# Kernel optimization log

Hardware: AMD Instinct MI355X
Metric: run time of the kernel (lower is better)

The kernel has to match this reference:

```python
import jax, jax.numpy as jnp
import numpy as np

N, P, D_IN, K, D_H = 4, 20000, 1024, 8, 64


def setup_inputs() -> dict:
    key = jax.random.key(0)
    ks = jax.random.split(key, 10)
    inp = {
        "x": jax.random.normal(ks[0], (N, P, D_IN), dtype=jnp.float32),
        "centroids": jax.random.normal(ks[1], (K, D_IN), dtype=jnp.float32),
        # proj_pre: Linear(in_dim, 64) + ReLU  (W stored as [in, out])
        "W_pre": jax.random.normal(ks[2], (D_IN, D_H), dtype=jnp.float32) / np.sqrt(D_IN),
        "b_pre": jnp.zeros((D_H,), dtype=jnp.float32),
        # attention: Linear(64,32) -> Tanh -> Linear(32,1)
        "W_a1": jax.random.normal(ks[3], (D_H, 32), dtype=jnp.float32) / np.sqrt(D_H),
        "b_a1": jnp.zeros((32,), dtype=jnp.float32),
        "W_a2": jax.random.normal(ks[4], (32, 1), dtype=jnp.float32) / np.sqrt(32.0),
        "b_a2": jnp.zeros((1,), dtype=jnp.float32),
        # proj_out: Linear(64,32) + ReLU (+ Dropout, identity at eval)
        "W_out": jax.random.normal(ks[5], (D_H, 32), dtype=jnp.float32) / np.sqrt(D_H),
        "b_out": jnp.zeros((32,), dtype=jnp.float32),
    }
    return inp


def reference(x, centroids, W_pre, b_pre, W_a1, b_a1, W_a2, b_a2, W_out, b_out):
    # --- cdist-based hard cluster assignment ---------------------------------
    # ||x - c||: use the expanded form to avoid an [n,p,K,d] broadcast.
    x2 = jnp.sum(x * x, axis=-1)                       # [n, p]
    c2 = jnp.sum(centroids * centroids, axis=-1)       # [K]
    d2 = x2[..., None] + c2 - 2.0 * jnp.einsum('npd,kd->npk', x, centroids)
    dist = jnp.sqrt(jnp.maximum(d2, 0.0))              # [n, p, K]

    wc = jax.nn.softmax(1e7 / dist, axis=-1)           # softmax(1e7/dist)
    wc = (wc > 0.5).astype(x.dtype)                    # hard assignment
    # F.normalize(p=1, dim=1): divide by per-(n,K) patch count (eps=1e-12)
    wc = wc / jnp.maximum(jnp.sum(wc, axis=1, keepdims=True), 1e-12)
    mask = jnp.sum(wc, axis=1) == 0                    # [n, K] empty clusters

    # --- per-patch projection -------------------------------------------------
    xp = jax.nn.relu(x @ W_pre + b_pre)                # [n, p, 64]

    # --- cluster pooling + attention ------------------------------------------
    x_cls = jnp.einsum('npd,nph->nhd', xp, wc)         # [n, K, 64]
    A = (jnp.tanh(x_cls @ W_a1 + b_a1) @ W_a2 + b_a2)[..., 0]  # [n, K]
    A = jnp.where(mask, jnp.asarray(-100000.0, A.dtype), A)
    wa = jax.nn.softmax(A, axis=-1)                    # [n, K]
    pooled = jnp.einsum('nhd,nh->nd', x_cls, wa)       # [n, 64]

    enc_cls = jax.nn.relu(pooled @ W_out + b_out)      # [n, 32] (dropout = eval)
    enc_seq = xp.reshape(-1, xp.shape[-1])             # [(n*p), 64]
    return enc_cls, enc_seq, enc_seq
```

## Files before the change

kernel.cpp:

```cpp
#include <hip/hip_runtime.h>
#include <math.h>

#define N_  4
#define P_  20000
#define DIN 1024
#define K_  8
#define DH  64
#define BP  128
#define NT  5

typedef float  f32x4 __attribute__((ext_vector_type(4)));
typedef short  s16x8 __attribute__((ext_vector_type(8)));
typedef unsigned int u32x4 __attribute__((ext_vector_type(4)));
typedef unsigned short ushort_t;


union FragU { u32x4 u; s16x8 s; };

__global__ __launch_bounds__(256) void k_prep(const float* __restrict__ W_pre,
                                              const float* __restrict__ centroids,
                                              float* __restrict__ ws) {
  const int c = blockIdx.x;
  const int t = threadIdx.x;
  ushort_t* Bth = (ushort_t*)(ws + 4096);
  ushort_t* Btl = (ushort_t*)(ws + 45056);
  for (int d = t; d < DIN; d += 256) {
    float v = 0.f;
    if (c < 64)      v = W_pre[(size_t)d * DH + c];
    else if (c < 72) v = centroids[(size_t)(c - 64) * DIN + d];
    unsigned u = __float_as_uint(v);
    unsigned r = u + 0x7FFFu + ((u >> 16) & 1u);
    unsigned hb = r & 0xFFFF0000u;
    float lo = v - __uint_as_float(hb);
    unsigned ul = __float_as_uint(lo);
    unsigned rl = ul + 0x7FFFu + ((ul >> 16) & 1u);
    Bth[(size_t)c * DIN + d] = (ushort_t)(hb >> 16);
    Btl[(size_t)c * DIN + d] = (ushort_t)(rl >> 16);
  }
}

__global__ __launch_bounds__(512) void k_init2(const float* __restrict__ centroids,
                                               float* __restrict__ ws) {
  const int t = threadIdx.x;
  int* gcnt = (int*)(ws + 2048);
  for (int i = t; i < N_ * K_ * DH; i += 512) ws[i] = 0.f;
  if (t < N_ * K_) gcnt[t] = 0;
  const int w = t >> 6, lane = t & 63;
  float s = 0.f;
  for (int d = lane; d < DIN; d += 64) {
    float v = centroids[(size_t)w * DIN + d];
    s += v * v;
  }
  for (int off = 32; off > 0; off >>= 1) s += __shfl_down(s, off, 64);
  if (lane == 0) ws[2080 + w] = s;
}

__global__ __launch_bounds__(256) void k_main(
    const float* __restrict__ x, const float* __restrict__ b_pre,
    float* __restrict__ out1, float* __restrict__ out2, float* __restrict__ ws) {
  __shared__ float xt[BP * 68];
  __shared__ float sc[BP * 9];
  __shared__ int   assign_s[BP];
  __shared__ int   cnt8[K_];
  __shared__ float c2s[K_];

  const int t = threadIdx.x;
  const int w = t >> 6, l = t & 63;
  const int n = blockIdx.y;
  const int p0 = blockIdx.x * BP;
  const int validP = (P_ - p0) < BP ? (P_ - p0) : BP;

  const ushort_t* Bth = (const ushort_t*)(ws + 4096);
  const ushort_t* Btl = (const ushort_t*)(ws + 45056);

  if (t < K_) { cnt8[t] = 0; c2s[t] = ws[2080 + t]; }

  f32x4 acc[2][NT];
#pragma unroll
  for (int rg = 0; rg < 2; ++rg)
#pragma unroll
    for (int tl = 0; tl < NT; ++tl) acc[rg][tl] = (f32x4){0.f, 0.f, 0.f, 0.f};

  const float* xbase = x + (size_t)n * P_ * DIN;
  const int quad8 = (l >> 4) << 3;

  for (int ch = 0; ch < 16; ++ch) {
    const int d0 = ch * 64;
    __syncthreads();
#pragma unroll
    for (int i = 0; i < 8; ++i) {
      const int idx = t + 256 * i;
      const int row = idx >> 4, c4 = (idx & 15) << 2;
      int gp = p0 + row; gp = gp < P_ ? gp : P_ - 1;
      f32x4 v = *(const f32x4*)(xbase + (size_t)gp * DIN + d0 + c4);
      *(f32x4*)(xt + row * 68 + c4) = v;
    }
    __syncthreads();

#pragma unroll
    for (int kk = 0; kk < 2; ++kk) {
      const int kb = d0 + kk * 32 + quad8;
      FragU bh[NT], bl[NT];
#pragma unroll
      for (int tl = 0; tl < NT; ++tl) {
        const size_t off = (size_t)(tl * 16 + (l & 15)) * DIN + kb;
        bh[tl].u = *(const u32x4*)(Bth + off);
        bl[tl].u = *(const u32x4*)(Btl + off);
      }
#pragma unroll
      for (int rg = 0; rg < 2; ++rg) {
        const int row = 32 * w + 16 * rg + (l & 15);
        const float* ap = xt + row * 68 + kk * 32 + quad8;
        f32x4 a0 = *(const f32x4*)ap;
        f32x4 a1 = *(const f32x4*)(ap + 4);
        float f[8];
#pragma unroll
        for (int e = 0; e < 4; ++e) { f[e] = a0[e]; f[4 + e] = a1[e]; }
        FragU ah, al;
#pragma unroll
        for (int q = 0; q < 4; ++q) {
          const unsigned u0 = __float_as_uint(f[2 * q]);
          const unsigned u1 = __float_as_uint(f[2 * q + 1]);
          ah.u[q] = (u0 >> 16) | (u1 & 0xFFFF0000u);
          const float l0 = f[2 * q]     - __uint_as_float(u0 & 0xFFFF0000u);
          const float l1 = f[2 * q + 1] - __uint_as_float(u1 & 0xFFFF0000u);
          al.u[q] = (__float_as_uint(l0) >> 16) | (__float_as_uint(l1) & 0xFFFF0000u);
        }
#pragma unroll
        for (int tl = 0; tl < NT; ++tl) {
          acc[rg][tl] = __builtin_amdgcn_mfma_f32_16x16x32_bf16(ah.s, bh[tl].s, acc[rg][tl], 0, 0, 0);
          acc[rg][tl] = __builtin_amdgcn_mfma_f32_16x16x32_bf16(ah.s, bl[tl].s, acc[rg][tl], 0, 0, 0);
          acc[rg][tl] = __builtin_amdgcn_mfma_f32_16x16x32_bf16(al.s, bh[tl].s, acc[rg][tl], 0, 0, 0);
        }
      }
    }
  }
  __syncthreads();

#pragma unroll
  for (int tl = 0; tl < 4; ++tl) {
    const int col = tl * 16 + (l & 15);
    const float bb = b_pre[col];
#pragma unroll
    for (int rg = 0; rg < 2; ++rg) {
#pragma unroll
      for (int r = 0; r < 4; ++r) {
        const int row = 32 * w + 16 * rg + ((l >> 4) << 2) + r;
        float v = acc[rg][tl][r] + bb;
        v = v > 0.f ? v : 0.f;
        xt[row * 65 + col] = v;
        if (row < validP) {
          const size_t o = (((size_t)(n * P_ + p0 + row)) << 6) + col;
          out1[o] = v;
          out2[o] = v;
        }
      }
    }
  }
  if ((l & 15) < K_) {
    const int k = l & 15;
#pragma unroll
    for (int rg = 0; rg < 2; ++rg)
#pragma unroll
      for (int r = 0; r < 4; ++r) {
        const int row = 32 * w + 16 * rg + ((l >> 4) << 2) + r;
        sc[row * 9 + k] = c2s[k] - 2.f * acc[rg][4][r];
      }
  }
  __syncthreads();

  if (t < BP) {
    int a = -1;
    if (t < validP) {
      float best = 3.4e38f; int bk = 0;
#pragma unroll
      for (int k = 0; k < K_; ++k) {
        const float v = sc[t * 9 + k];
        if (v < best) { best = v; bk = k; }
      }
      a = bk;
      atomicAdd(&cnt8[bk], 1);
    }
    assign_s[t] = a;
  }
  __syncthreads();

  for (int task = t; task < K_ * DH; task += 256) {
    const int k = task >> 6, j = task & 63;
    float s = 0.f;
    for (int p = 0; p < BP; ++p)
      s += (assign_s[p] == k) ? xt[p * 65 + j] : 0.f;
    if (s != 0.f) atomicAdd(&ws[(n * K_ + k) * DH + j], s);
  }
  if (t < K_ && cnt8[t] > 0) atomicAdd((int*)(ws + 2048) + n * K_ + t, cnt8[t]);
}

__global__ __launch_bounds__(256) void k_final(
    const float* __restrict__ W_a1, const float* __restrict__ b_a1,
    const float* __restrict__ W_a2, const float* __restrict__ b_a2,
    const float* __restrict__ W_out, const float* __restrict__ b_out,
    const float* __restrict__ ws, float* __restrict__ enc_cls) {
  __shared__ float xc[N_ * K_ * DH];
  __shared__ float wa[N_ * K_];
  __shared__ float As[N_ * K_];
  __shared__ int   cnts[N_ * K_];
  __shared__ float pooled[N_ * DH];
  const int t = threadIdx.x;
  const float* gsum = ws;
  const int* gcnt = (const int*)(ws + 2048);

  if (t < N_ * K_) cnts[t] = gcnt[t];
  __syncthreads();
  for (int i = t; i < N_ * K_ * DH; i += 256) {
    const int nk = i >> 6;
    const int c = cnts[nk];
    xc[i] = (c > 0) ? gsum[i] / (float)c : 0.f;
  }
  __syncthreads();
  if (t < N_ * K_) {
    float a = b_a2[0];
    for (int h = 0; h < 32; ++h) {
      float z = b_a1[h];
      for (int j = 0; j < DH; ++j) z += xc[t * DH + j] * W_a1[j * 32 + h];
      a += tanhf(z) * W_a2[h];
    }
    As[t] = (cnts[t] > 0) ? a : -100000.f;
  }
  __syncthreads();
  if (t < N_) {
    float m = -3.4e38f;
    for (int k = 0; k < K_; ++k) m = fmaxf(m, As[t * K_ + k]);
    float ssum = 0.f;
    float e[K_];
    for (int k = 0; k < K_; ++k) { e[k] = expf(As[t * K_ + k] - m); ssum += e[k]; }
    for (int k = 0; k < K_; ++k) wa[t * K_ + k] = e[k] / ssum;
  }
  __syncthreads();
  {
    const int n = t >> 6, j = t & 63;
    float s = 0.f;
    for (int k = 0; k < K_; ++k) s += xc[(n * K_ + k) * DH + j] * wa[n * K_ + k];
    pooled[t] = s;
  }
  __syncthreads();
  if (t < N_ * 32) {
    const int n = t >> 5, o = t & 31;
    float s = b_out[o];
    for (int j = 0; j < DH; ++j) s += pooled[n * DH + j] * W_out[j * 32 + o];
    enc_cls[n * 32 + o] = fmaxf(s, 0.f);
  }
}

extern "C" void kernel_launch(void* const* d_in, const int* in_sizes, int n_in,
                              void* d_out, int out_size, void* d_ws, size_t ws_size,
                              hipStream_t stream) {
  const float* x         = (const float*)d_in[0];
  const float* centroids = (const float*)d_in[1];
  const float* W_pre     = (const float*)d_in[2];
  const float* b_pre     = (const float*)d_in[3];
  const float* W_a1      = (const float*)d_in[4];
  const float* b_a1      = (const float*)d_in[5];
  const float* W_a2      = (const float*)d_in[6];
  const float* b_a2      = (const float*)d_in[7];
  const float* W_out     = (const float*)d_in[8];
  const float* b_out     = (const float*)d_in[9];

  float* out     = (float*)d_out;
  float* ws      = (float*)d_ws;
  float* enc_cls = out;
  float* out1    = out + N_ * 32;
  float* out2    = out + N_ * 32 + (size_t)N_ * P_ * DH;

  hipLaunchKernelGGL(k_prep, dim3(80), dim3(256), 0, stream, W_pre, centroids, ws);
  hipLaunchKernelGGL(k_init2, dim3(1), dim3(512), 0, stream, centroids, ws);
  hipLaunchKernelGGL(k_main, dim3((P_ + BP - 1) / BP, N_), dim3(256), 0, stream,
                     x, b_pre, out1, out2, ws);
  hipLaunchKernelGGL(k_final, dim3(1), dim3(256), 0, stream,
                     W_a1, b_a1, W_a2, b_a2, W_out, b_out, ws, enc_cls);
}
```

Before: 620.1 us.

## Double-buffer x tiles via async global-to-LDS loads with XOR swizzle

The main kernel now stages each 64-column chunk of x into shared memory with global_load_lds direct copies into two alternating buffers. The next chunk is issued before the MFMA work on the current one, so global loads overlap compute and the register round trip plus one barrier per chunk go away. The padded layout is replaced by an XOR swizzle to avoid LDS bank conflicts. The two small setup kernels are also merged into one launch. Correctness depends on the barrier waiting for the outstanding LDS-DMA loads, and the doubled shared-memory footprint may lower occupancy.

New measurement: 589.6 us. 1.05x faster.

```diff
diff --git a/kernel.cpp b/kernel.cpp
--- a/kernel.cpp
+++ b/kernel.cpp
@@ -17,48 +17,53 @@
 
 union FragU { u32x4 u; s16x8 s; };
 
-__global__ __launch_bounds__(256) void k_prep(const float* __restrict__ W_pre,
-                                              const float* __restrict__ centroids,
-                                              float* __restrict__ ws) {
-  const int c = blockIdx.x;
+__device__ __forceinline__ void async_ld16(const float* g, float* l) {
+  __builtin_amdgcn_global_load_lds(
+      (const __attribute__((address_space(1))) unsigned int*)g,
+      (__attribute__((address_space(3))) unsigned int*)l, 16, 0, 0);
+}
+
+__global__ __launch_bounds__(512) void k_pre(const float* __restrict__ W_pre,
+                                             const float* __restrict__ centroids,
+                                             float* __restrict__ ws) {
   const int t = threadIdx.x;
-  ushort_t* Bth = (ushort_t*)(ws + 4096);
-  ushort_t* Btl = (ushort_t*)(ws + 45056);
-  for (int d = t; d < DIN; d += 256) {
-    float v = 0.f;
-    if (c < 64)      v = W_pre[(size_t)d * DH + c];
-    else if (c < 72) v = centroids[(size_t)(c - 64) * DIN + d];
-    unsigned u = __float_as_uint(v);
-    unsigned r = u + 0x7FFFu + ((u >> 16) & 1u);
-    unsigned hb = r & 0xFFFF0000u;
-    float lo = v - __uint_as_float(hb);
-    unsigned ul = __float_as_uint(lo);
-    unsigned rl = ul + 0x7FFFu + ((ul >> 16) & 1u);
-    Bth[(size_t)c * DIN + d] = (ushort_t)(hb >> 16);
-    Btl[(size_t)c * DIN + d] = (ushort_t)(rl >> 16);
-  }
-}
-
-__global__ __launch_bounds__(512) void k_init2(const float* __restrict__ centroids,
-                                               float* __restrict__ ws) {
-  const int t = threadIdx.x;
-  int* gcnt = (int*)(ws + 2048);
-  for (int i = t; i < N_ * K_ * DH; i += 512) ws[i] = 0.f;
-  if (t < N_ * K_) gcnt[t] = 0;
-  const int w = t >> 6, lane = t & 63;
-  float s = 0.f;
-  for (int d = lane; d < DIN; d += 64) {
-    float v = centroids[(size_t)w * DIN + d];
-    s += v * v;
-  }
-  for (int off = 32; off > 0; off >>= 1) s += __shfl_down(s, off, 64);
-  if (lane == 0) ws[2080 + w] = s;
+  const int b = blockIdx.x;
+  if (b < 80) {
+    const int c = b;
+    ushort_t* Bth = (ushort_t*)(ws + 4096);
+    ushort_t* Btl = (ushort_t*)(ws + 45056);
+    for (int d = t; d < DIN; d += 512) {
+      float v = 0.f;
+      if (c < 64)      v = W_pre[(size_t)d * DH + c];
+      else if (c < 72) v = centroids[(size_t)(c - 64) * DIN + d];
+      unsigned u = __float_as_uint(v);
+      unsigned r = u + 0x7FFFu + ((u >> 16) & 1u);
+      unsigned hb = r & 0xFFFF0000u;
+      float lo = v - __uint_as_float(hb);
+      unsigned ul = __float_as_uint(lo);
+      unsigned rl = ul + 0x7FFFu + ((ul >> 16) & 1u);
+      Bth[(size_t)c * DIN + d] = (ushort_t)(hb >> 16);
+      Btl[(size_t)c * DIN + d] = (ushort_t)(rl >> 16);
+    }
+  } else {
+    int* gcnt = (int*)(ws + 2048);
+    for (int i = t; i < N_ * K_ * DH; i += 512) ws[i] = 0.f;
+    if (t < N_ * K_) gcnt[t] = 0;
+    const int w = t >> 6, lane = t & 63;
+    float s = 0.f;
+    for (int d = lane; d < DIN; d += 64) {
+      float v = centroids[(size_t)w * DIN + d];
+      s += v * v;
+    }
+    for (int off = 32; off > 0; off >>= 1) s += __shfl_down(s, off, 64);
+    if (lane == 0) ws[2080 + w] = s;
+  }
 }
 
 __global__ __launch_bounds__(256) void k_main(
     const float* __restrict__ x, const float* __restrict__ b_pre,
     float* __restrict__ out1, float* __restrict__ out2, float* __restrict__ ws) {
-  __shared__ float xt[BP * 68];
+  __shared__ float smem[2 * BP * 64];
   __shared__ float sc[BP * 9];
   __shared__ int   assign_s[BP];
   __shared__ int   cnt8[K_];
@@ -66,6 +71,8 @@
 
   const int t = threadIdx.x;
   const int w = t >> 6, l = t & 63;
+  const int m = l & 15, q4 = l >> 4;
+  const int quad8 = q4 << 3;
   const int n = blockIdx.y;
   const int p0 = blockIdx.x * BP;
   const int validP = (P_ - p0) < BP ? (P_ - p0) : BP;
@@ -82,37 +89,48 @@
     for (int tl = 0; tl < NT; ++tl) acc[rg][tl] = (f32x4){0.f, 0.f, 0.f, 0.f};
 
   const float* xbase = x + (size_t)n * P_ * DIN;
-  const int quad8 = (l >> 4) << 3;
+
+  const float* gsrc[8];
+  float* ldst[8];
+#pragma unroll
+  for (int ii = 0; ii < 8; ++ii) {
+    const int R = w * 32 + ii * 4;
+    const int row = R + q4;
+    const int g = m ^ (row & 15);
+    int gp = p0 + row; gp = gp < P_ ? gp : P_ - 1;
+    gsrc[ii] = xbase + (size_t)gp * DIN + 4 * g;
+    ldst[ii] = smem + R * 64;
+  }
+
+#pragma unroll
+  for (int ii = 0; ii < 8; ++ii) async_ld16(gsrc[ii], ldst[ii]);
 
   for (int ch = 0; ch < 16; ++ch) {
-    const int d0 = ch * 64;
     __syncthreads();
-#pragma unroll
-    for (int i = 0; i < 8; ++i) {
-      const int idx = t + 256 * i;
-      const int row = idx >> 4, c4 = (idx & 15) << 2;
-      int gp = p0 + row; gp = gp < P_ ? gp : P_ - 1;
-      f32x4 v = *(const f32x4*)(xbase + (size_t)gp * DIN + d0 + c4);
-      *(f32x4*)(xt + row * 68 + c4) = v;
-    }
-    __syncthreads();
+    if (ch < 15) {
+      const int nb = (ch + 1) & 1;
+#pragma unroll
+      for (int ii = 0; ii < 8; ++ii)
+        async_ld16(gsrc[ii] + (ch + 1) * 64, ldst[ii] + nb * 8192);
+    }
+    const float* bufp = smem + (ch & 1) * 8192;
 
 #pragma unroll
     for (int kk = 0; kk < 2; ++kk) {
-      const int kb = d0 + kk * 32 + quad8;
+      const int kb = ch * 64 + kk * 32 + quad8;
       FragU bh[NT], bl[NT];
 #pragma unroll
       for (int tl = 0; tl < NT; ++tl) {
-        const size_t off = (size_t)(tl * 16 + (l & 15)) * DIN + kb;
+        const size_t off = (size_t)(tl * 16 + m) * DIN + kb;
         bh[tl].u = *(const u32x4*)(Bth + off);
         bl[tl].u = *(const u32x4*)(Btl + off);
       }
 #pragma unroll
       for (int rg = 0; rg < 2; ++rg) {
-        const int row = 32 * w + 16 * rg + (l & 15);
-        const float* ap = xt + row * 68 + kk * 32 + quad8;
-        f32x4 a0 = *(const f32x4*)ap;
-        f32x4 a1 = *(const f32x4*)(ap + 4);
+        const int row = 32 * w + 16 * rg + m;
+        const int ga = kk * 8 + (q4 << 1);
+        f32x4 a0 = *(const f32x4*)(bufp + row * 64 + 4 * (ga ^ m));
+        f32x4 a1 = *(const f32x4*)(bufp + row * 64 + 4 * ((ga + 1) ^ m));
         float f[8];
 #pragma unroll
         for (int e = 0; e < 4; ++e) { f[e] = a0[e]; f[4 + e] = a1[e]; }
@@ -139,16 +157,16 @@
 
 #pragma unroll
   for (int tl = 0; tl < 4; ++tl) {
-    const int col = tl * 16 + (l & 15);
+    const int col = tl * 16 + m;
     const float bb = b_pre[col];
 #pragma unroll
     for (int rg = 0; rg < 2; ++rg) {
 #pragma unroll
       for (int r = 0; r < 4; ++r) {
-        const int row = 32 * w + 16 * rg + ((l >> 4) << 2) + r;
+        const int row = 32 * w + 16 * rg + (q4 << 2) + r;
         float v = acc[rg][tl][r] + bb;
         v = v > 0.f ? v : 0.f;
-        xt[row * 65 + col] = v;
+        smem[row * 65 + col] = v;
         if (row < validP) {
           const size_t o = (((size_t)(n * P_ + p0 + row)) << 6) + col;
           out1[o] = v;
@@ -157,14 +175,13 @@
       }
     }
   }
-  if ((l & 15) < K_) {
-    const int k = l & 15;
+  if (m < K_) {
 #pragma unroll
     for (int rg = 0; rg < 2; ++rg)
 #pragma unroll
       for (int r = 0; r < 4; ++r) {
-        const int row = 32 * w + 16 * rg + ((l >> 4) << 2) + r;
-        sc[row * 9 + k] = c2s[k] - 2.f * acc[rg][4][r];
+        const int row = 32 * w + 16 * rg + (q4 << 2) + r;
+        sc[row * 9 + m] = c2s[m] - 2.f * acc[rg][4][r];
       }
   }
   __syncthreads();
@@ -189,7 +206,7 @@
     const int k = task >> 6, j = task & 63;
     float s = 0.f;
     for (int p = 0; p < BP; ++p)
-      s += (assign_s[p] == k) ? xt[p * 65 + j] : 0.f;
+      s += (assign_s[p] == k) ? smem[p * 65 + j] : 0.f;
     if (s != 0.f) atomicAdd(&ws[(n * K_ + k) * DH + j], s);
   }
   if (t < K_ && cnt8[t] > 0) atomicAdd((int*)(ws + 2048) + n * K_ + t, cnt8[t]);
@@ -228,11 +245,11 @@
   }
   __syncthreads();
   if (t < N_) {
-    float m = -3.4e38f;
-    for (int k = 0; k < K_; ++k) m = fmaxf(m, As[t * K_ + k]);
+    float mx = -3.4e38f;
+    for (int k = 0; k < K_; ++k) mx = fmaxf(mx, As[t * K_ + k]);
     float ssum = 0.f;
     float e[K_];
-    for (int k = 0; k < K_; ++k) { e[k] = expf(As[t * K_ + k] - m); ssum += e[k]; }
+    for (int k = 0; k < K_; ++k) { e[k] = expf(As[t * K_ + k] - mx); ssum += e[k]; }
     for (int k = 0; k < K_; ++k) wa[t * K_ + k] = e[k] / ssum;
   }
   __syncthreads();
@@ -271,8 +288,7 @@
   float* out1    = out + N_ * 32;
   float* out2    = out + N_ * 32 + (size_t)N_ * P_ * DH;
 
-  hipLaunchKernelGGL(k_prep, dim3(80), dim3(256), 0, stream, W_pre, centroids, ws);
-  hipLaunchKernelGGL(k_init2, dim3(1), dim3(512), 0, stream, centroids, ws);
+  hipLaunchKernelGGL(k_pre, dim3(81), dim3(512), 0, stream, W_pre, centroids, ws);
   hipLaunchKernelGGL(k_main, dim3((P_ + BP - 1) / BP, N_), dim3(256), 0, stream,
                      x, b_pre, out1, out2, ws);
   hipLaunchKernelGGL(k_final, dim3(1), dim3(256), 0, stream,
```
